# Kernel optimization log

Hardware: AMD Instinct MI355X
Metric: run time of the kernel (lower is better)

The kernel has to match this reference:

```python
import jax, jax.numpy as jnp
import numpy as np

K = 0.1            # manifold curvature param: points satisfy <x,x>_L = -1/K
H = 8              # num_heads
DH = 64            # head_spatial_dim
SP = 512           # spatial_dim = H*DH
SCALE = 1.0 / np.sqrt(DH)
SQRT_K = np.sqrt(K).astype(np.float32)


def _lorentz_fc(x, W, b):
    # Manifold-constrained FC: linear map to spatial coords, time recomputed
    sp = x @ W + b                                            # [..., out_spatial]
    t = jnp.sqrt(jnp.clip(1.0 / K + jnp.sum(sp * sp, axis=-1, keepdims=True), 1e-9, None))
    return jnp.concatenate([t, sp], axis=-1)


def _logmap0(p):
    # Lorentz log map at origin -> tangent spatial coords (time comp = 0)
    t, sp = p[..., :1], p[..., 1:]
    nrm = jnp.sqrt(jnp.sum(sp * sp, axis=-1, keepdims=True))
    theta = jnp.arccosh(jnp.clip(SQRT_K * t, 1.0 + 1e-7, None))
    return (theta / SQRT_K) * sp / jnp.maximum(nrm, 1e-9)


def _expmap0(u):
    nrm = jnp.sqrt(jnp.sum(u * u, axis=-1, keepdims=True))
    t = jnp.cosh(SQRT_K * nrm) / SQRT_K
    sp = jnp.sinh(SQRT_K * nrm) * u / (SQRT_K * jnp.maximum(nrm, 1e-9))
    return jnp.concatenate([t, sp], axis=-1)


def setup_inputs() -> dict:
    key = jax.random.key(0)
    ks = jax.random.split(key, 9)
    B, N = 4, 2048
    space = jax.random.normal(ks[0], (B, N, SP), dtype=jnp.float32) * 0.5
    t = jnp.sqrt(1.0 / K + jnp.sum(space * space, axis=-1, keepdims=True))
    x = jnp.concatenate([t, space], axis=-1)                  # on-manifold [B,N,513]
    s = (1 + SP) ** -0.5
    Wq = jax.random.normal(ks[1], (1 + SP, SP), dtype=jnp.float32) * s
    Wk = jax.random.normal(ks[2], (1 + SP, SP), dtype=jnp.float32) * s
    Wv = jax.random.normal(ks[3], (1 + SP, SP), dtype=jnp.float32) * s
    Wo = jax.random.normal(ks[4], (1 + SP, SP), dtype=jnp.float32) * s
    bq = jax.random.normal(ks[5], (SP,), dtype=jnp.float32) * 0.01
    bk = jax.random.normal(ks[6], (SP,), dtype=jnp.float32) * 0.01
    bv = jax.random.normal(ks[7], (SP,), dtype=jnp.float32) * 0.01
    bo = jax.random.normal(ks[8], (SP,), dtype=jnp.float32) * 0.01
    return {"x": x, "Wq": Wq, "bq": bq, "Wk": Wk, "bk": bk, "Wv": Wv, "bv": bv, "Wo": Wo, "bo": bo}


def _split_heads(p):
    # [B,N,1+H*DH] -> [B,H,N,1+DH], sharing the time component across heads
    B, N, _ = p.shape
    t = p[..., :1]                                            # [B,N,1]
    sp = p[..., 1:].reshape(B, N, H, DH)
    t = jnp.broadcast_to(t[:, :, None, :], (B, N, H, 1))
    return jnp.concatenate([t, sp], axis=-1).transpose(0, 2, 1, 3)


def reference(x, Wq, bq, Wk, bk, Wv, bv, Wo, bo):
    q = _split_heads(_lorentz_fc(x, Wq, bq))                  # [B,H,N,1+DH]
    k = _split_heads(_lorentz_fc(x, Wk, bk))
    v = _split_heads(_lorentz_fc(x, Wv, bv))
    # Lorentzian inner product scores: -q_t k_t + <q_s, k_s>
    scores = (jnp.einsum('bhnd,bhmd->bhnm', q[..., 1:], k[..., 1:])
              - jnp.einsum('bhni,bhmi->bhnm', q[..., :1], k[..., :1])) * SCALE
    attn = jax.nn.softmax(scores, axis=-1)                    # [B,H,N,N]
    # Riemannian aggregation: logmap0 -> weighted sum in tangent space -> expmap0
    v_tan = _logmap0(v)                                       # [B,H,N,DH]
    out_tan = jnp.einsum('bhnm,bhmd->bhnd', attn, v_tan)
    out = _expmap0(out_tan)                                   # [B,H,N,1+DH]
    # direct head concat: stack spatial parts, renormalize time onto manifold
    B, _, N, _ = out.shape
    space_cat = out[..., 1:].transpose(0, 2, 1, 3).reshape(B, N, H * DH)
    t_prime = jnp.sqrt(jnp.clip(1.0 / K + jnp.sum(space_cat * space_cat, axis=-1, keepdims=True), 1e-9, None))
    cat = jnp.concatenate([t_prime, space_cat], axis=-1)      # [B,N,513]
    return _lorentz_fc(cat, Wo, bo)                           # [B,N,513]
```

## Files before the change

kernel.cpp:

```cpp
#include <hip/hip_runtime.h>
#include <math.h>

#define H_    8
#define DH_   64
#define SPD   512
#define NSEQ  2048
#define BATCH 4
#define ROWS  8192
#define KDIM  513
#define KPAD  544
#define INVK  10.0f
#define SQRTK 0.31622776601683794f
#define S2C   0.18033688011112043f
#define LOG2E 1.4426950408889634f
#define TKOFF 12.0f

using bf16x8 = __attribute__((ext_vector_type(8))) short;
using f32x4  = __attribute__((ext_vector_type(4))) float;
using f32x16 = __attribute__((ext_vector_type(16))) float;

static __device__ __forceinline__ short f2bf(float f){
  union { float f; unsigned u; } v; v.f = f;
  unsigned r = v.u + 0x7fffu + ((v.u >> 16) & 1u);
  return (short)(r >> 16);
}
static __device__ __forceinline__ float bf2f(short s){
  union { unsigned u; float f; } v; v.u = ((unsigned)(unsigned short)s) << 16;
  return v.f;
}
static __device__ __forceinline__ unsigned cvtpk(float lo, float hi){
  unsigned r; asm("v_cvt_pk_bf16_f32 %0, %1, %2" : "=v"(r) : "v"(lo), "v"(hi)); return r;
}
static __device__ __forceinline__ void plswapf(float& a, float& b){
  asm("v_permlane32_swap_b32 %0, %1" : "+v"(a), "+v"(b));
}
static __device__ __forceinline__ void plswapu(unsigned& a, unsigned& b){
  asm("v_permlane32_swap_b32 %0, %1" : "+v"(a), "+v"(b));
}
static __device__ __forceinline__ float exp2v(float x){
  float r; asm("v_exp_f32 %0, %1" : "=v"(r) : "v"(x)); return r;
}

#define GL16(gp, lp) __builtin_amdgcn_global_load_lds( \
    (const __attribute__((address_space(1))) void*)(gp), \
    (__attribute__((address_space(3))) void*)(lp), 16, 0, 0)

__global__ __launch_bounds__(256) void convx_kernel(const float* __restrict__ x,
                                                    short* __restrict__ xb){
  int i = blockIdx.x * 256 + threadIdx.x;
  if (i >= ROWS * KPAD) return;
  int r = i / KPAD, c = i - r * KPAD;
  xb[i] = (c < KDIM) ? f2bf(x[(size_t)r * KDIM + c]) : (short)0;
}

__global__ __launch_bounds__(256) void convw_kernel(const float* __restrict__ Wq,
                                                    const float* __restrict__ Wk,
                                                    const float* __restrict__ Wv,
                                                    const float* __restrict__ Wo,
                                                    short* __restrict__ WT){
  int wsel = blockIdx.y;
  const float* W = (wsel == 0) ? Wq : (wsel == 1) ? Wk : (wsel == 2) ? Wv : Wo;
  int i = blockIdx.x * 256 + threadIdx.x;
  if (i >= SPD * KPAD) return;
  int n = i / KPAD, k = i - n * KPAD;
  WT[(size_t)wsel * SPD * KPAD + i] = (k < KDIM) ? f2bf(W[(size_t)k * SPD + n]) : (short)0;
}

template<bool BF16OUT, int BM>
__global__ __launch_bounds__(256) void gemm_kernel(
    const short* __restrict__ A, const short* __restrict__ WTbase,
    int sel0, int sel1, int sel2,
    const float* __restrict__ bias0, const float* __restrict__ bias1,
    const float* __restrict__ bias2,
    void* __restrict__ C0, void* __restrict__ C1, void* __restrict__ C2,
    int ldc, int coff)
{
  constexpr int NREP = (BM == 128) ? 4 : 2;
  const int z = blockIdx.z;
  const int sel = (z == 0) ? sel0 : (z == 1) ? sel1 : sel2;
  const short* BT = WTbase + (size_t)sel * SPD * KPAD;
  const float* bias = (z == 0) ? bias0 : (z == 1) ? bias1 : bias2;
  void* C = (z == 0) ? C0 : (z == 1) ? C1 : C2;

  __shared__ short As[BM * 32];
  __shared__ short Bs[128 * 32];

  const int tid  = threadIdx.x;
  const int lane = tid & 63;
  const int wave = tid >> 6;
  const int row0 = blockIdx.x * BM;
  const int col0 = blockIdx.y * 128;
  const int wr = (BM == 128) ? (wave >> 1) * 64 : 0;
  const int wc = (BM == 128) ? (wave & 1) * 64 : wave * 32;
  const int rA  = lane & 15;
  const int kg2 = (lane >> 4) * 16;

  f32x4 acc[4][NREP] = {};

  for (int kt = 0; kt < KPAD / 32; ++kt){
    __syncthreads();
    #pragma unroll
    for (int p = 0; p < BM / 64; ++p){
      const int idx = p * 256 + tid;
      const int r = idx >> 2, c4 = idx & 3;
      const int gc = (c4 ^ ((r >> 1) & 3)) * 8;
      GL16(A + (size_t)(row0 + r) * KPAD + kt * 32 + gc, (char*)As + idx * 16);
    }
    #pragma unroll
    for (int p = 0; p < 2; ++p){
      const int idx = p * 256 + tid;
      const int r = idx >> 2, c4 = idx & 3;
      const int gc = (c4 ^ ((r >> 1) & 3)) * 8;
      GL16(BT + (size_t)(col0 + r) * KPAD + kt * 32 + gc, (char*)Bs + idx * 16);
    }
    asm volatile("s_waitcnt vmcnt(0)" ::: "memory");
    __syncthreads();
    bf16x8 af[4], bfr[NREP];
    #pragma unroll
    for (int m = 0; m < 4; ++m){
      const int r = wr + m * 16 + rA;
      af[m] = *(const bf16x8*)((const char*)As + ((r * 64 + kg2) ^ (((r >> 1) & 3) << 4)));
    }
    #pragma unroll
    for (int n = 0; n < NREP; ++n){
      const int r = wc + n * 16 + rA;
      bfr[n] = *(const bf16x8*)((const char*)Bs + ((r * 64 + kg2) ^ (((r >> 1) & 3) << 4)));
    }
    #pragma unroll
    for (int m = 0; m < 4; ++m)
      #pragma unroll
      for (int n = 0; n < NREP; ++n)
        acc[m][n] = __builtin_amdgcn_mfma_f32_16x16x32_bf16(af[m], bfr[n], acc[m][n], 0, 0, 0);
  }

  #pragma unroll
  for (int m = 0; m < 4; ++m){
    const int row = row0 + wr + m * 16 + (lane >> 4) * 4;
    #pragma unroll
    for (int n = 0; n < NREP; ++n){
      const int col = col0 + wc + n * 16 + rA;
      const float bv = bias[col];
      #pragma unroll
      for (int j = 0; j < 4; ++j){
        const float v = acc[m][n][j] + bv;
        if (BF16OUT) ((short*)C)[(size_t)(row + j) * SPD + col] = f2bf(v);
        else         ((float*)C)[(size_t)(row + j) * ldc + coff + col] = v;
      }
    }
  }
}

__global__ __launch_bounds__(256) void postqkv_kernel(
    const short* __restrict__ qb, const short* __restrict__ kb,
    const short* __restrict__ vb, float* __restrict__ tq,
    unsigned* __restrict__ tkpk, short* __restrict__ vtT)
{
  const int tid = threadIdx.x;
  const int lane = tid & 63;
  const int wv = tid >> 6;
  const int row0 = blockIdx.x * 8 + wv * 2;
  const int b = blockIdx.x >> 8;

  #pragma unroll
  for (int i = 0; i < 2; ++i){
    const int row = row0 + i;
    const int n = row & (NSEQ - 1);
    {
      union { bf16x8 v; short e[8]; } u;
      u.v = *(const bf16x8*)(qb + (size_t)row * SPD + lane * 8);
      float s = 0.f;
      #pragma unroll
      for (int j = 0; j < 8; ++j){ const float f = bf2f(u.e[j]); s += f * f; }
      #pragma unroll
      for (int m = 1; m <= 32; m <<= 1) s += __shfl_xor(s, m, 64);
      if (lane == 0) tq[row] = sqrtf(INVK + s);
    }
    {
      union { bf16x8 v; short e[8]; } u;
      u.v = *(const bf16x8*)(kb + (size_t)row * SPD + lane * 8);
      float s = 0.f;
      #pragma unroll
      for (int j = 0; j < 8; ++j){ const float f = bf2f(u.e[j]); s += f * f; }
      #pragma unroll
      for (int m = 1; m <= 32; m <<= 1) s += __shfl_xor(s, m, 64);
      if (lane == 0){
        const float tkm = sqrtf(INVK + s) - TKOFF;
        const short bhi = f2bf(tkm);
        const short blo = f2bf(tkm - bf2f(bhi));
        tkpk[row] = (unsigned)(unsigned short)bhi | ((unsigned)(unsigned short)blo << 16);
      }
    }
    {
      union { bf16x8 v; short e[8]; } u;
      u.v = *(const bf16x8*)(vb + (size_t)row * SPD + lane * 8);
      float f[8]; float sh = 0.f;
      #pragma unroll
      for (int j = 0; j < 8; ++j){ f[j] = bf2f(u.e[j]); sh += f[j] * f[j]; }
      sh += __shfl_xor(sh, 1, 64);
      sh += __shfl_xor(sh, 2, 64);
      sh += __shfl_xor(sh, 4, 64);
      float tot = sh;
      tot += __shfl_xor(tot, 8, 64);
      tot += __shfl_xor(tot, 16, 64);
      tot += __shfl_xor(tot, 32, 64);
      const float tv = sqrtf(INVK + tot);
      const float av = fmaxf(SQRTK * tv, 1.0f + 1e-7f);
      const float theta = __logf(av + sqrtf(av * av - 1.0f));
      const float fac = theta * (1.0f / SQRTK);
      const float inv = fac / fmaxf(sqrtf(sh), 1e-9f);
      const int h = lane >> 3;
      const int d0 = (lane & 7) * 8;
      short* dst = vtT + ((size_t)((b * H_ + h) * DH_ + d0)) * NSEQ + n;
      #pragma unroll
      for (int j = 0; j < 8; ++j) dst[(size_t)j * NSEQ] = f2bf(inv * f[j]);
    }
  }
}

__global__ __launch_bounds__(256) void attn_kernel(
    const short* __restrict__ qb, const short* __restrict__ kb,
    const short* __restrict__ vtT, const float* __restrict__ tqg,
    const unsigned* __restrict__ tkpk, short* __restrict__ catb)
{
  int bid = blockIdx.x;
  bid = (bid & 7) * 64 + (bid >> 3);
  const int qt = bid & 15;
  const int bh = bid >> 4;
  const int b = bh >> 3, h = bh & 7;
  const int q0 = qt * 128;
  const int tid = threadIdx.x;
  const int lane = tid & 63;
  const int w = tid >> 6;
  const int l31 = lane & 31;
  const int hi = lane >> 5;
  const int rsw = (l31 & 7) << 4;

  __shared__ short Ks[2][64 * 64];
  __shared__ short Vs[2][64 * 64];
  __shared__ float lred[4][32];
  __shared__ unsigned tks[NSEQ];

  const int qrow = q0 + w * 32 + l31;
  bf16x8 qf[4];
  {
    const short* qptr = qb + (size_t)(b * NSEQ + qrow) * SPD + h * DH_ + hi * 8;
    #pragma unroll
    for (int s = 0; s < 4; ++s){
      union { bf16x8 v; short e[8]; } u;
      u.v = *(const bf16x8*)(qptr + s * 16);
      #pragma unroll
      for (int j = 0; j < 8; ++j) u.e[j] = f2bf(bf2f(u.e[j]) * S2C);
      qf[s] = u.v;
    }
  }
  bf16x8 qf4;
  {
    const float a = -S2C * tqg[b * NSEQ + qrow];
    const short ahi = f2bf(a);
    const short alo = f2bf(a - bf2f(ahi));
    union { unsigned u[4]; bf16x8 v; } q4;
    q4.u[0] = hi ? 0u : ((unsigned)(unsigned short)ahi | ((unsigned)(unsigned short)alo << 16));
    q4.u[1] = hi ? 0u : (unsigned)(unsigned short)ahi;
    q4.u[2] = 0; q4.u[3] = 0;
    qf4 = q4.v;
  }

  {
    const unsigned* tsrc = tkpk + b * NSEQ + tid * 8;
    *(uint4*)&tks[tid * 8]     = *(const uint4*)tsrc;
    *(uint4*)&tks[tid * 8 + 4] = *(const uint4*)(tsrc + 4);
  }

  const int rB = tid >> 3;
  const int c0 = (tid & 7) * 16;
  const int cc = c0 ^ ((rB & 7) << 4);
  const short* kbase = kb + (size_t)(b * NSEQ) * SPD + h * DH_;
  const short* vbase = vtT + (size_t)(bh * DH_) * NSEQ;

  uint4 kA0, kA1, vA0, vA1;
  uint4 kB0, kB1, vB0, vB1;

#define LOADA(m0) do{ \
    kA0 = *(const uint4*)(kbase + (size_t)((m0) + rB) * SPD + (c0 >> 1)); \
    kA1 = *(const uint4*)(kbase + (size_t)((m0) + 32 + rB) * SPD + (c0 >> 1)); \
    vA0 = *(const uint4*)(vbase + (size_t)rB * NSEQ + (m0) + (c0 >> 1)); \
    vA1 = *(const uint4*)(vbase + (size_t)(32 + rB) * NSEQ + (m0) + (c0 >> 1)); }while(0)
#define LOADB(m0) do{ \
    kB0 = *(const uint4*)(kbase + (size_t)((m0) + rB) * SPD + (c0 >> 1)); \
    kB1 = *(const uint4*)(kbase + (size_t)((m0) + 32 + rB) * SPD + (c0 >> 1)); \
    vB0 = *(const uint4*)(vbase + (size_t)rB * NSEQ + (m0) + (c0 >> 1)); \
    vB1 = *(const uint4*)(vbase + (size_t)(32 + rB) * NSEQ + (m0) + (c0 >> 1)); }while(0)
#define WRITEA(buf) do{ \
    *(uint4*)((char*)Ks[buf] + rB * 128 + cc) = kA0; \
    *(uint4*)((char*)Ks[buf] + (32 + rB) * 128 + cc) = kA1; \
    *(uint4*)((char*)Vs[buf] + rB * 128 + cc) = vA0; \
    *(uint4*)((char*)Vs[buf] + (32 + rB) * 128 + cc) = vA1; }while(0)
#define WRITEB(buf) do{ \
    *(uint4*)((char*)Ks[buf] + rB * 128 + cc) = kB0; \
    *(uint4*)((char*)Ks[buf] + (32 + rB) * 128 + cc) = kB1; \
    *(uint4*)((char*)Vs[buf] + rB * 128 + cc) = vB0; \
    *(uint4*)((char*)Vs[buf] + (32 + rB) * 128 + cc) = vB1; }while(0)
#define BARRIER() asm volatile("s_waitcnt lgkmcnt(0)\n\ts_barrier" ::: "memory")
#define WAITV4()  asm volatile("s_waitcnt vmcnt(4)" ::: "memory")
#define WAITV0()  asm volatile("s_waitcnt vmcnt(0)" ::: "memory")

  float l_run = 0.f;
  f32x16 o[2] = {};

  auto KAUG = [&](unsigned pk)->bf16x8{
    union { unsigned u[4]; bf16x8 v; } ka;
    ka.u[0] = hi ? 0u : ((pk & 0xFFFFu) | (pk << 16));
    ka.u[1] = hi ? 0u : (pk >> 16);
    ka.u[2] = 0; ka.u[3] = 0;
    return ka.v;
  };

  auto COMPUTE = [&](const char* Kc, const char* Vc, int m0){
    const unsigned pk0 = tks[m0 + l31];
    const unsigned pk1 = tks[m0 + 32 + l31];

    f32x16 sacc[2] = {};
    __builtin_amdgcn_s_setprio(1);
    #pragma unroll
    for (int f = 0; f < 2; ++f){
      const int rowb = (f * 32 + l31) * 128;
      #pragma unroll
      for (int s = 0; s < 4; ++s){
        const bf16x8 kf = *(const bf16x8*)(Kc + rowb + ((s * 32 + hi * 16) ^ rsw));
        sacc[f] = __builtin_amdgcn_mfma_f32_32x32x16_bf16(kf, qf[s], sacc[f], 0, 0, 0);
      }
    }
    sacc[0] = __builtin_amdgcn_mfma_f32_32x32x16_bf16(KAUG(pk0), qf4, sacc[0], 0, 0, 0);
    sacc[1] = __builtin_amdgcn_mfma_f32_32x32x16_bf16(KAUG(pk1), qf4, sacc[1], 0, 0, 0);
    __builtin_amdgcn_s_setprio(0);

    #pragma unroll
    for (int f = 0; f < 2; ++f)
      #pragma unroll
      for (int e = 0; e < 16; ++e)
        sacc[f][e] = exp2v(sacc[f][e]);

    float s16[16];
    #pragma unroll
    for (int e = 0; e < 16; ++e) s16[e] = sacc[0][e] + sacc[1][e];
    #pragma unroll
    for (int st = 8; st; st >>= 1)
      #pragma unroll
      for (int e = 0; e < st; ++e) s16[e] += s16[e + st];
    float rs = s16[0];
    { float ca = rs, cb = rs; plswapf(ca, cb); rs += hi ? ca : cb; }
    l_run += rs;

    bf16x8 pa[4];
    #pragma unroll
    for (int f = 0; f < 2; ++f)
      #pragma unroll
      for (int g16 = 0; g16 < 2; ++g16){
        const int bse = g16 * 8;
        unsigned A0 = cvtpk(sacc[f][bse + 0], sacc[f][bse + 1]);
        unsigned A1 = cvtpk(sacc[f][bse + 2], sacc[f][bse + 3]);
        unsigned B0 = cvtpk(sacc[f][bse + 4], sacc[f][bse + 5]);
        unsigned B1 = cvtpk(sacc[f][bse + 6], sacc[f][bse + 7]);
        plswapu(A0, B0);
        plswapu(A1, B1);
        union { unsigned u[4]; bf16x8 v; } pu;
        pu.u[0] = A0; pu.u[1] = A1; pu.u[2] = B0; pu.u[3] = B1;
        pa[f * 2 + g16] = pu.v;
      }

    __builtin_amdgcn_s_setprio(1);
    #pragma unroll
    for (int db = 0; db < 2; ++db){
      const int rowb = (db * 32 + l31) * 128;
      #pragma unroll
      for (int ks = 0; ks < 4; ++ks){
        const bf16x8 vf = *(const bf16x8*)(Vc + rowb + ((ks * 32 + hi * 16) ^ rsw));
        o[db] = __builtin_amdgcn_mfma_f32_32x32x16_bf16(pa[ks], vf, o[db], 0, 0, 0);
      }
    }
    __builtin_amdgcn_s_setprio(0);
  };

  LOADA(0);
  WAITV0();
  WRITEA(0);
  __syncthreads();
  LOADB(64);

  const int NT = NSEQ / 64;
  #pragma unroll 1
  for (int t = 0; t < NT; t += 2){
    const int m0 = t * 64;
    if (t + 2 < NT) LOADA(m0 + 128);
    COMPUTE((const char*)Ks[0], (const char*)Vs[0], m0);
    if (t + 2 < NT) WAITV4(); else WAITV0();
    WRITEB(1);
    BARRIER();
    if (t + 3 < NT) LOADB(m0 + 192);
    COMPUTE((const char*)Ks[1], (const char*)Vs[1], m0 + 64);
    if (t + 2 < NT){
      if (t + 3 < NT) WAITV4(); else WAITV0();
      WRITEA(0);
    }
    BARRIER();
  }

  if (lane < 32) lred[w][l31] = l_run;
  asm volatile("s_waitcnt lgkmcnt(0)" ::: "memory");
  f32x4 lv[4];
  #pragma unroll
  for (int g = 0; g < 4; ++g) lv[g] = *(const f32x4*)&lred[w][8 * g + 4 * hi];

  const size_t obase = (size_t)(b * NSEQ + q0 + w * 32) * KPAD + 1 + h * DH_ + l31;
  #pragma unroll
  for (int e = 0; e < 16; ++e){
    const float linv = __builtin_amdgcn_rcpf(lv[e >> 2][e & 3]);
    const float ov0 = o[0][e] * linv;
    const float ov1 = o[1][e] * linv;
    float ss = ov0 * ov0 + ov1 * ov1;
    #pragma unroll
    for (int off = 16; off; off >>= 1) ss += __shfl_xor(ss, off, 64);
    const float nrm = sqrtf(ss);
    const float e2 = exp2f(SQRTK * nrm * LOG2E);
    const float einv = __builtin_amdgcn_rcpf(e2);
    const float fac = (e2 - einv) * 0.5f * __builtin_amdgcn_rcpf(SQRTK * fmaxf(nrm, 1e-9f));
    const int crow = (e & 3) + 8 * (e >> 2) + 4 * hi;
    catb[obase + (size_t)crow * KPAD]      = f2bf(fac * ov0);
    catb[obase + (size_t)crow * KPAD + 32] = f2bf(fac * ov1);
  }
#undef LOADA
#undef LOADB
#undef WRITEA
#undef WRITEB
#undef BARRIER
#undef WAITV4
#undef WAITV0
}

__global__ __launch_bounds__(512) void tprime_kernel(short* __restrict__ catb){
  const int row = blockIdx.x;
  const int t = threadIdx.x, lane = t & 63, w = t >> 6;
  __shared__ float red[8];
  float v = bf2f(catb[(size_t)row * KPAD + 1 + t]);
  float s = v * v;
  #pragma unroll
  for (int m = 32; m; m >>= 1) s += __shfl_xor(s, m, 64);
  if (lane == 0) red[w] = s;
  __syncthreads();
  float tot = 0.f;
  #pragma unroll
  for (int i = 0; i < 8; ++i) tot += red[i];
  if (t == 0) catb[(size_t)row * KPAD] = f2bf(sqrtf(fmaxf(INVK + tot, 1e-9f)));
  if (t < KPAD - KDIM) catb[(size_t)row * KPAD + KDIM + t] = 0;
}

__global__ __launch_bounds__(512) void finalize_kernel(float* __restrict__ out){
  const int row = blockIdx.x;
  const int t = threadIdx.x, lane = t & 63, w = t >> 6;
  __shared__ float red[8];
  float v = out[(size_t)row * KDIM + 1 + t];
  float s = v * v;
  #pragma unroll
  for (int m = 32; m; m >>= 1) s += __shfl_xor(s, m, 64);
  if (lane == 0) red[w] = s;
  __syncthreads();
  float tot = 0.f;
  #pragma unroll
  for (int i = 0; i < 8; ++i) tot += red[i];
  if (t == 0) out[(size_t)row * KDIM] = sqrtf(fmaxf(INVK + tot, 1e-9f));
}

extern "C" void kernel_launch(void* const* d_in, const int* in_sizes, int n_in,
                              void* d_out, int out_size, void* d_ws, size_t ws_size,
                              hipStream_t stream)
{
  (void)in_sizes; (void)n_in; (void)out_size; (void)ws_size;
  const float* x  = (const float*)d_in[0];
  const float* Wq = (const float*)d_in[1];
  const float* bq = (const float*)d_in[2];
  const float* Wk = (const float*)d_in[3];
  const float* bk = (const float*)d_in[4];
  const float* Wv = (const float*)d_in[5];
  const float* bv = (const float*)d_in[6];
  const float* Wo = (const float*)d_in[7];
  const float* bo = (const float*)d_in[8];
  float* out = (float*)d_out;

  char* p = (char*)d_ws;
  short* xb   = (short*)p; p += (size_t)ROWS * KPAD * 2;
  short* WT   = (short*)p; p += (size_t)4 * SPD * KPAD * 2;
  short* qb   = (short*)p; p += (size_t)ROWS * SPD * 2;
  short* kb   = (short*)p; p += (size_t)ROWS * SPD * 2;
  short* vb   = (short*)p; p += (size_t)ROWS * SPD * 2;
  short* vtT  = (short*)p; p += (size_t)ROWS * SPD * 2;
  float* tq   = (float*)p; p += (size_t)ROWS * 4;
  unsigned* tkpk = (unsigned*)p; p += (size_t)ROWS * 4;
  short* catb = (short*)p; p += (size_t)ROWS * KPAD * 2;

  convx_kernel<<<(ROWS * KPAD) / 256, 256, 0, stream>>>(x, xb);
  convw_kernel<<<dim3((SPD * KPAD + 255) / 256, 4), 256, 0, stream>>>(Wq, Wk, Wv, Wo, WT);
  gemm_kernel<true, 128><<<dim3(64, 4, 3), 256, 0, stream>>>(
      xb, WT, 0, 1, 2, bq, bk, bv, qb, kb, vb, SPD, 0);
  postqkv_kernel<<<1024, 256, 0, stream>>>(qb, kb, vb, tq, tkpk, vtT);
  attn_kernel<<<512, 256, 0, stream>>>(qb, kb, vtT, tq, tkpk, catb);
  tprime_kernel<<<ROWS, 512, 0, stream>>>(catb);
  gemm_kernel<false, 64><<<dim3(128, 4, 1), 256, 0, stream>>>(
      catb, WT, 3, 3, 3, bo, bo, bo, out, out, out, KDIM, 1);
  finalize_kernel<<<ROWS, 512, 0, stream>>>(out);
}
```

Measured before the change: 158.9 us.

## Split time column out of GEMMs as rank-1 epilogue, compute row sums via MFMA

Drops the padded K=544 layout. The GEMMs now run over K=512 spatial columns only, and the time-component contribution is added in the epilogue as t_row*W[0,col]. This cuts the K loop from 17 to 16 tiles and shrinks the conversion buffers. The softmax row-sum is moved from a VALU reduction tree plus permlane swap into extra MFMAs against a ones vector. The tprime and finalize reductions are rewritten to use one wave per row, and tprime no longer writes into catb.

Result: faster. 146.4 us (-7.9%).

```diff
diff --git a/kernel.cpp b/kernel.cpp
--- a/kernel.cpp
+++ b/kernel.cpp
@@ -8,7 +8,6 @@
 #define BATCH 4
 #define ROWS  8192
 #define KDIM  513
-#define KPAD  544
 #define INVK  10.0f
 #define SQRTK 0.31622776601683794f
 #define S2C   0.18033688011112043f
@@ -31,9 +30,6 @@
 static __device__ __forceinline__ unsigned cvtpk(float lo, float hi){
   unsigned r; asm("v_cvt_pk_bf16_f32 %0, %1, %2" : "=v"(r) : "v"(lo), "v"(hi)); return r;
 }
-static __device__ __forceinline__ void plswapf(float& a, float& b){
-  asm("v_permlane32_swap_b32 %0, %1" : "+v"(a), "+v"(b));
-}
 static __device__ __forceinline__ void plswapu(unsigned& a, unsigned& b){
   asm("v_permlane32_swap_b32 %0, %1" : "+v"(a), "+v"(b));
 }
@@ -46,11 +42,14 @@
     (__attribute__((address_space(3))) void*)(lp), 16, 0, 0)
 
 __global__ __launch_bounds__(256) void convx_kernel(const float* __restrict__ x,
-                                                    short* __restrict__ xb){
-  int i = blockIdx.x * 256 + threadIdx.x;
-  if (i >= ROWS * KPAD) return;
-  int r = i / KPAD, c = i - r * KPAD;
-  xb[i] = (c < KDIM) ? f2bf(x[(size_t)r * KDIM + c]) : (short)0;
+                                                    short* __restrict__ xs){
+  const int i2 = (blockIdx.x * 256 + threadIdx.x) * 2;
+  const int r = i2 >> 9, c = i2 & 511;
+  const float a = x[(size_t)r * KDIM + 1 + c];
+  const float b = x[(size_t)r * KDIM + 2 + c];
+  const unsigned pk = (unsigned)(unsigned short)f2bf(a) |
+                      ((unsigned)(unsigned short)f2bf(b) << 16);
+  *(unsigned*)(xs + (size_t)r * SPD + c) = pk;
 }
 
 __global__ __launch_bounds__(256) void convw_kernel(const float* __restrict__ Wq,
@@ -58,12 +57,11 @@
                                                     const float* __restrict__ Wv,
                                                     const float* __restrict__ Wo,
                                                     short* __restrict__ WT){
-  int wsel = blockIdx.y;
+  const int wsel = blockIdx.y;
   const float* W = (wsel == 0) ? Wq : (wsel == 1) ? Wk : (wsel == 2) ? Wv : Wo;
-  int i = blockIdx.x * 256 + threadIdx.x;
-  if (i >= SPD * KPAD) return;
-  int n = i / KPAD, k = i - n * KPAD;
-  WT[(size_t)wsel * SPD * KPAD + i] = (k < KDIM) ? f2bf(W[(size_t)k * SPD + n]) : (short)0;
+  const int i = blockIdx.x * 256 + threadIdx.x;
+  const int n = i >> 9, k = i & 511;
+  WT[(size_t)wsel * SPD * SPD + i] = f2bf(W[(size_t)(k + 1) * SPD + n]);
 }
 
 template<bool BF16OUT, int BM>
@@ -72,14 +70,18 @@
     int sel0, int sel1, int sel2,
     const float* __restrict__ bias0, const float* __restrict__ bias1,
     const float* __restrict__ bias2,
+    const float* __restrict__ W00, const float* __restrict__ W01,
+    const float* __restrict__ W02,
+    const float* __restrict__ tvec, long tstride,
     void* __restrict__ C0, void* __restrict__ C1, void* __restrict__ C2,
     int ldc, int coff)
 {
   constexpr int NREP = (BM == 128) ? 4 : 2;
   const int z = blockIdx.z;
   const int sel = (z == 0) ? sel0 : (z == 1) ? sel1 : sel2;
-  const short* BT = WTbase + (size_t)sel * SPD * KPAD;
+  const short* BT = WTbase + (size_t)sel * SPD * SPD;
   const float* bias = (z == 0) ? bias0 : (z == 1) ? bias1 : bias2;
+  const float* W0 = (z == 0) ? W00 : (z == 1) ? W01 : W02;
   void* C = (z == 0) ? C0 : (z == 1) ? C1 : C2;
 
   __shared__ short As[BM * 32];
@@ -94,24 +96,25 @@
   const int wc = (BM == 128) ? (wave & 1) * 64 : wave * 32;
   const int rA  = lane & 15;
   const int kg2 = (lane >> 4) * 16;
+  const int g4  = lane >> 4;
 
   f32x4 acc[4][NREP] = {};
 
-  for (int kt = 0; kt < KPAD / 32; ++kt){
+  for (int kt = 0; kt < SPD / 32; ++kt){
     __syncthreads();
     #pragma unroll
     for (int p = 0; p < BM / 64; ++p){
       const int idx = p * 256 + tid;
       const int r = idx >> 2, c4 = idx & 3;
       const int gc = (c4 ^ ((r >> 1) & 3)) * 8;
-      GL16(A + (size_t)(row0 + r) * KPAD + kt * 32 + gc, (char*)As + idx * 16);
+      GL16(A + (size_t)(row0 + r) * SPD + kt * 32 + gc, (char*)As + idx * 16);
     }
     #pragma unroll
     for (int p = 0; p < 2; ++p){
       const int idx = p * 256 + tid;
       const int r = idx >> 2, c4 = idx & 3;
       const int gc = (c4 ^ ((r >> 1) & 3)) * 8;
-      GL16(BT + (size_t)(col0 + r) * KPAD + kt * 32 + gc, (char*)Bs + idx * 16);
+      GL16(BT + (size_t)(col0 + r) * SPD + kt * 32 + gc, (char*)Bs + idx * 16);
     }
     asm volatile("s_waitcnt vmcnt(0)" ::: "memory");
     __syncthreads();
@@ -133,16 +136,24 @@
         acc[m][n] = __builtin_amdgcn_mfma_f32_16x16x32_bf16(af[m], bfr[n], acc[m][n], 0, 0, 0);
   }
 
+  float trow[4][4];
+  #pragma unroll
+  for (int m = 0; m < 4; ++m)
+    #pragma unroll
+    for (int j = 0; j < 4; ++j)
+      trow[m][j] = tvec[(size_t)(row0 + wr + m * 16 + g4 * 4 + j) * tstride];
+
   #pragma unroll
   for (int m = 0; m < 4; ++m){
-    const int row = row0 + wr + m * 16 + (lane >> 4) * 4;
+    const int row = row0 + wr + m * 16 + g4 * 4;
     #pragma unroll
     for (int n = 0; n < NREP; ++n){
       const int col = col0 + wc + n * 16 + rA;
       const float bv = bias[col];
+      const float w0 = W0[col];
       #pragma unroll
       for (int j = 0; j < 4; ++j){
-        const float v = acc[m][n][j] + bv;
+        const float v = acc[m][n][j] + trow[m][j] * w0 + bv;
         if (BF16OUT) ((short*)C)[(size_t)(row + j) * SPD + col] = f2bf(v);
         else         ((float*)C)[(size_t)(row + j) * ldc + coff + col] = v;
       }
@@ -263,6 +274,13 @@
     q4.u[1] = hi ? 0u : (unsigned)(unsigned short)ahi;
     q4.u[2] = 0; q4.u[3] = 0;
     qf4 = q4.v;
+  }
+  bf16x8 onesB;
+  {
+    const unsigned val = (l31 == 0) ? 0x3f803f80u : 0u;
+    union { unsigned u[4]; bf16x8 v; } ob;
+    ob.u[0] = val; ob.u[1] = val; ob.u[2] = val; ob.u[3] = val;
+    onesB = ob.v;
   }
 
   {
@@ -304,8 +322,8 @@
 #define WAITV4()  asm volatile("s_waitcnt vmcnt(4)" ::: "memory")
 #define WAITV0()  asm volatile("s_waitcnt vmcnt(0)" ::: "memory")
 
-  float l_run = 0.f;
   f32x16 o[2] = {};
+  f32x16 lacc = {};
 
   auto KAUG = [&](unsigned pk)->bf16x8{
     union { unsigned u[4]; bf16x8 v; } ka;
@@ -339,17 +357,6 @@
       #pragma unroll
       for (int e = 0; e < 16; ++e)
         sacc[f][e] = exp2v(sacc[f][e]);
-
-    float s16[16];
-    #pragma unroll
-    for (int e = 0; e < 16; ++e) s16[e] = sacc[0][e] + sacc[1][e];
-    #pragma unroll
-    for (int st = 8; st; st >>= 1)
-      #pragma unroll
-      for (int e = 0; e < st; ++e) s16[e] += s16[e + st];
-    float rs = s16[0];
-    { float ca = rs, cb = rs; plswapf(ca, cb); rs += hi ? ca : cb; }
-    l_run += rs;
 
     bf16x8 pa[4];
     #pragma unroll
@@ -378,6 +385,9 @@
         o[db] = __builtin_amdgcn_mfma_f32_32x32x16_bf16(pa[ks], vf, o[db], 0, 0, 0);
       }
     }
+    #pragma unroll
+    for (int ks = 0; ks < 4; ++ks)
+      lacc = __builtin_amdgcn_mfma_f32_32x32x16_bf16(pa[ks], onesB, lacc, 0, 0, 0);
     __builtin_amdgcn_s_setprio(0);
   };
 
@@ -405,13 +415,17 @@
     BARRIER();
   }
 
-  if (lane < 32) lred[w][l31] = l_run;
+  if (l31 == 0){
+    #pragma unroll
+    for (int e = 0; e < 16; ++e)
+      lred[w][(e & 3) + 8 * (e >> 2) + 4 * hi] = lacc[e];
+  }
   asm volatile("s_waitcnt lgkmcnt(0)" ::: "memory");
   f32x4 lv[4];
   #pragma unroll
   for (int g = 0; g < 4; ++g) lv[g] = *(const f32x4*)&lred[w][8 * g + 4 * hi];
 
-  const size_t obase = (size_t)(b * NSEQ + q0 + w * 32) * KPAD + 1 + h * DH_ + l31;
+  const size_t obase = (size_t)(b * NSEQ + q0 + w * 32) * SPD + h * DH_ + l31;
   #pragma unroll
   for (int e = 0; e < 16; ++e){
     const float linv = __builtin_amdgcn_rcpf(lv[e >> 2][e & 3]);
@@ -425,8 +439,8 @@
     const float einv = __builtin_amdgcn_rcpf(e2);
     const float fac = (e2 - einv) * 0.5f * __builtin_amdgcn_rcpf(SQRTK * fmaxf(nrm, 1e-9f));
     const int crow = (e & 3) + 8 * (e >> 2) + 4 * hi;
-    catb[obase + (size_t)crow * KPAD]      = f2bf(fac * ov0);
-    catb[obase + (size_t)crow * KPAD + 32] = f2bf(fac * ov1);
+    catb[obase + (size_t)crow * SPD]      = f2bf(fac * ov0);
+    catb[obase + (size_t)crow * SPD + 32] = f2bf(fac * ov1);
   }
 #undef LOADA
 #undef LOADB
@@ -437,37 +451,30 @@
 #undef WAITV0
 }
 
-__global__ __launch_bounds__(512) void tprime_kernel(short* __restrict__ catb){
-  const int row = blockIdx.x;
-  const int t = threadIdx.x, lane = t & 63, w = t >> 6;
-  __shared__ float red[8];
-  float v = bf2f(catb[(size_t)row * KPAD + 1 + t]);
-  float s = v * v;
-  #pragma unroll
-  for (int m = 32; m; m >>= 1) s += __shfl_xor(s, m, 64);
-  if (lane == 0) red[w] = s;
-  __syncthreads();
-  float tot = 0.f;
-  #pragma unroll
-  for (int i = 0; i < 8; ++i) tot += red[i];
-  if (t == 0) catb[(size_t)row * KPAD] = f2bf(sqrtf(fmaxf(INVK + tot, 1e-9f)));
-  if (t < KPAD - KDIM) catb[(size_t)row * KPAD + KDIM + t] = 0;
-}
-
-__global__ __launch_bounds__(512) void finalize_kernel(float* __restrict__ out){
-  const int row = blockIdx.x;
-  const int t = threadIdx.x, lane = t & 63, w = t >> 6;
-  __shared__ float red[8];
-  float v = out[(size_t)row * KDIM + 1 + t];
-  float s = v * v;
-  #pragma unroll
-  for (int m = 32; m; m >>= 1) s += __shfl_xor(s, m, 64);
-  if (lane == 0) red[w] = s;
-  __syncthreads();
-  float tot = 0.f;
-  #pragma unroll
-  for (int i = 0; i < 8; ++i) tot += red[i];
-  if (t == 0) out[(size_t)row * KDIM] = sqrtf(fmaxf(INVK + tot, 1e-9f));
+__global__ __launch_bounds__(256) void tp_kernel(const short* __restrict__ catb,
+                                                 float* __restrict__ tps){
+  const int lane = threadIdx.x & 63;
+  const int row = blockIdx.x * 4 + (threadIdx.x >> 6);
+  union { bf16x8 v; short e[8]; } u;
+  u.v = *(const bf16x8*)(catb + (size_t)row * SPD + lane * 8);
+  float s = 0.f;
+  #pragma unroll
+  for (int j = 0; j < 8; ++j){ const float f = bf2f(u.e[j]); s += f * f; }
+  #pragma unroll
+  for (int m = 1; m <= 32; m <<= 1) s += __shfl_xor(s, m, 64);
+  if (lane == 0) tps[row] = sqrtf(fmaxf(INVK + s, 1e-9f));
+}
+
+__global__ __launch_bounds__(256) void fin_kernel(float* __restrict__ out){
+  const int lane = threadIdx.x & 63;
+  const int row = blockIdx.x * 4 + (threadIdx.x >> 6);
+  const float* rp = out + (size_t)row * KDIM + 1;
+  float s = 0.f;
+  #pragma unroll
+  for (int j = 0; j < 8; ++j){ const float f = rp[j * 64 + lane]; s += f * f; }
+  #pragma unroll
+  for (int m = 1; m <= 32; m <<= 1) s += __shfl_xor(s, m, 64);
+  if (lane == 0) out[(size_t)row * KDIM] = sqrtf(fmaxf(INVK + s, 1e-9f));
 }
 
 extern "C" void kernel_launch(void* const* d_in, const int* in_sizes, int n_in,
@@ -487,24 +494,27 @@
   float* out = (float*)d_out;
 
   char* p = (char*)d_ws;
-  short* xb   = (short*)p; p += (size_t)ROWS * KPAD * 2;
-  short* WT   = (short*)p; p += (size_t)4 * SPD * KPAD * 2;
+  short* xs   = (short*)p; p += (size_t)ROWS * SPD * 2;
+  short* WT   = (short*)p; p += (size_t)4 * SPD * SPD * 2;
   short* qb   = (short*)p; p += (size_t)ROWS * SPD * 2;
   short* kb   = (short*)p; p += (size_t)ROWS * SPD * 2;
   short* vb   = (short*)p; p += (size_t)ROWS * SPD * 2;
   short* vtT  = (short*)p; p += (size_t)ROWS * SPD * 2;
   float* tq   = (float*)p; p += (size_t)ROWS * 4;
   unsigned* tkpk = (unsigned*)p; p += (size_t)ROWS * 4;
-  short* catb = (short*)p; p += (size_t)ROWS * KPAD * 2;
-
-  convx_kernel<<<(ROWS * KPAD) / 256, 256, 0, stream>>>(x, xb);
-  convw_kernel<<<dim3((SPD * KPAD + 255) / 256, 4), 256, 0, stream>>>(Wq, Wk, Wv, Wo, WT);
+  short* catb = (short*)p; p += (size_t)ROWS * SPD * 2;
+  float* tps  = (float*)p; p += (size_t)ROWS * 4;
+
+  convx_kernel<<<(ROWS * SPD / 2) / 256, 256, 0, stream>>>(x, xs);
+  convw_kernel<<<dim3((SPD * SPD) / 256, 4), 256, 0, stream>>>(Wq, Wk, Wv, Wo, WT);
   gemm_kernel<true, 128><<<dim3(64, 4, 3), 256, 0, stream>>>(
-      xb, WT, 0, 1, 2, bq, bk, bv, qb, kb, vb, SPD, 0);
+      xs, WT, 0, 1, 2, bq, bk, bv, Wq, Wk, Wv, x, (long)KDIM,
+      qb, kb, vb, SPD, 0);
   postqkv_kernel<<<1024, 256, 0, stream>>>(qb, kb, vb, tq, tkpk, vtT);
   attn_kernel<<<512, 256, 0, stream>>>(qb, kb, vtT, tq, tkpk, catb);
-  tprime_kernel<<<ROWS, 512, 0, stream>>>(catb);
+  tp_kernel<<<ROWS / 4, 256, 0, stream>>>(catb, tps);
   gemm_kernel<false, 64><<<dim3(128, 4, 1), 256, 0, stream>>>(
-      catb, WT, 3, 3, 3, bo, bo, bo, out, out, out, KDIM, 1);
-  finalize_kernel<<<ROWS, 512, 0, stream>>>(out);
-}
+      catb, WT, 3, 3, 3, bo, bo, bo, Wo, Wo, Wo, tps, 1L,
+      out, out, out, KDIM, 1);
+  fin_kernel<<<ROWS / 4, 256, 0, stream>>>(out);
+}
```
